# Optimization experiments

Measured on AMD Instinct MI355X. Metric: run time of the kernel, lower is better.

## Reference

```python
import jax, jax.numpy as jnp
import numpy as np

N_Q = 8
DIM = 128
CODEBOOK_SIZE = 1024


def setup_inputs() -> dict:
    key = jax.random.key(0)
    k1, k2 = jax.random.split(key)
    x = jax.random.normal(k1, (8, DIM, 4096), dtype=jnp.float32)
    codebooks = jax.random.normal(k2, (N_Q, CODEBOOK_SIZE, DIM), dtype=jnp.float32)
    return {"x": x, "codebooks": codebooks, "frame_rate": 75}


def _rvq(xt, codebooks):
    # xt: (B, T, D); codebooks: (n_q, K, D)
    def stage(carry, cb):
        residual, qout = carry
        # squared euclidean distance (B, T, K); argmin == Encodec's argmax of -dist
        d = (jnp.sum(residual * residual, axis=-1, keepdims=True)
             - 2.0 * jnp.einsum('btd,kd->btk', residual, cb)
             + jnp.sum(cb * cb, axis=-1))
        idx = jnp.argmin(d, axis=-1)                     # (B, T)
        q = cb[idx]                                       # gather: (B, T, D)
        # commit loss: mse(quantize.detach(), input)
        commit = jnp.mean((jax.lax.stop_gradient(q) - residual) ** 2)
        # straight-through estimator
        q_st = residual + jax.lax.stop_gradient(q - residual)
        return (residual - q_st, qout + q_st), (idx, commit)

    init = (xt, jnp.zeros_like(xt))
    (_, qout), (codes, commits) = jax.lax.scan(stage, init, codebooks)
    return qout, codes, commits


def reference(x, codebooks, frame_rate):
    # x: (B, D, T) -> (B, T, D)
    xt = jnp.swapaxes(x, 1, 2)
    qout, codes, commits = _rvq(xt, codebooks)
    quantized = jnp.swapaxes(qout, 1, 2)                 # (B, D, T)
    n_q, K, _ = codebooks.shape
    bw_per_q = np.log2(K) * frame_rate
    bw = jnp.asarray(n_q * bw_per_q, dtype=jnp.float32)
    penalty = jnp.mean(commits)
    return quantized, codes, bw, penalty
```

## Files before the change

kernel.cpp:

```cpp
#include <hip/hip_runtime.h>
#include <math.h>

#define Bsz 8
#define Dd  128
#define Tt  4096
#define Kk  1024
#define NQ  8
#define BT  (Bsz*Tt)
#define MT  128
#define NTHR 512
#define WV  8
#define DELTA 0.05f

typedef float f32x4 __attribute__((ext_vector_type(4)));
typedef short short8 __attribute__((ext_vector_type(8)));

__device__ __forceinline__ unsigned short f2bf(float x) {
    unsigned u = __float_as_uint(x);
    u += 0x7FFF + ((u >> 16) & 1);
    return (unsigned short)(u >> 16);
}
__device__ __forceinline__ float bf2f(unsigned short h) {
    return __uint_as_float(((unsigned)h) << 16);
}

__device__ __forceinline__ void gload_lds16(const void* g, void* l) {
    __builtin_amdgcn_global_load_lds(
        (const __attribute__((address_space(1))) unsigned int*)g,
        (__attribute__((address_space(3))) unsigned int*)l, 16, 0, 0);
}

__global__ void k_init(const float* __restrict__ x,
                       float* __restrict__ resid) {
    __shared__ float tile[32][33];
    int b  = blockIdx.z;
    int t0 = blockIdx.x * 32, d0 = blockIdx.y * 32;
    int tx = threadIdx.x, ty = threadIdx.y;
    #pragma unroll
    for (int k = 0; k < 4; k++) {
        int d = d0 + ty + k * 8;
        tile[ty + k * 8][tx] = x[((size_t)(b * Dd + d)) * Tt + t0 + tx];
    }
    __syncthreads();
    #pragma unroll
    for (int k = 0; k < 4; k++) {
        int t = t0 + ty + k * 8;
        resid[((size_t)(b * Tt + t)) * Dd + d0 + tx] = tile[tx][ty + k * 8];
    }
}

__global__ void k_prep(const float* __restrict__ cb, char* __restrict__ bswz) {
    int ln = threadIdx.x;
    int kc = blockIdx.x & 3;
    int t  = (blockIdx.x >> 2) & 63;
    int q  = blockIdx.x >> 8;
    int code = t * 16 + (ln & 15);
    int d0   = kc * 32 + (ln >> 4) * 8;
    const float* src = cb + ((size_t)(q * Kk + code)) * Dd + d0;
    float v[8];
    *(float4*)&v[0] = *(const float4*)src;
    *(float4*)&v[4] = *(const float4*)(src + 4);
    short8 h, l;
    #pragma unroll
    for (int j = 0; j < 8; j++) {
        unsigned short hu = f2bf(v[j]);
        h[j] = (short)hu;
        l[j] = (short)f2bf(v[j] - bf2f(hu));
    }
    char* base = bswz + ((size_t)(q * 64 + t)) * 8192;
    *(short8*)(base + kc * 1024 + ln * 16) = h;
    *(short8*)(base + 4096 + kc * 1024 + ln * 16) = l;
}

__global__ void k_c2(const float* __restrict__ cb,
                     float* __restrict__ c2,
                     double* __restrict__ commits) {
    int row  = blockIdx.x * 4 + (threadIdx.x >> 6);
    int lane = threadIdx.x & 63;
    const float* p = cb + (size_t)row * Dd;
    float a = p[lane], b = p[lane + 64];
    float s = a * a + b * b;
    #pragma unroll
    for (int off = 32; off; off >>= 1) s += __shfl_down(s, off);
    if (lane == 0) c2[row] = s;
    if (blockIdx.x == 0 && threadIdx.x < NQ) commits[threadIdx.x] = 0.0;
}

__device__ __forceinline__ float exact_score_sw(const float* __restrict__ rldsb,
                                                int p,
                                                const float* __restrict__ crow,
                                                float c2v) {
    const f32x4* r4 = (const f32x4*)rldsb;
    const f32x4* c4 = (const f32x4*)crow;
    int rb = p * 32, sw = p & 7;
    float a = 0.0f;
    #pragma unroll
    for (int d4 = 0; d4 < 32; d4++) {
        f32x4 r = r4[rb + (d4 ^ sw)];
        f32x4 c = c4[d4];
        a = fmaf(r[0], c[0], a); a = fmaf(r[1], c[1], a);
        a = fmaf(r[2], c[2], a); a = fmaf(r[3], c[3], a);
    }
    return fmaf(-2.0f, a, c2v);
}

__global__ __launch_bounds__(NTHR, 2) void k_rvq_fused(
        float* __restrict__ resid,
        const float* __restrict__ cb,
        const char*  __restrict__ bswz,
        const float* __restrict__ c2g,
        float* __restrict__ codes_f,
        double* __restrict__ commits) {
    __shared__ float rlds[MT * Dd];
    __shared__ float c2s[Kk];
    __shared__ f32x4 bbuf[2][2][512];
    __shared__ float fA1[MT], fA2[MT], fA3[MT];
    __shared__ float fB1[MT], fB2[MT], fB3[MT];
    __shared__ int   iA1[MT], iA2[MT], iB1[MT], iB2[MT];
    __shared__ int   sidxs[MT];
    __shared__ int   nfall, flist[MT];
    __shared__ float fwv[WV]; __shared__ int fwi[WV];
    __shared__ float csum[WV];

    const int tid  = threadIdx.x;
    const int w    = tid >> 6, ln = tid & 63;
    const int quad = ln >> 4,  m  = ln & 15;
    const int wg   = w & 3,    half = w >> 2;
    const int toff = half * 32;
    const int base = blockIdx.x * MT;
    const int prow0 = wg * 32 + m;
    const int prow1 = wg * 32 + 16 + m;

    f32x4* r4 = (f32x4*)rlds;

    {
        const f32x4* src = (const f32x4*)(resid + (size_t)base * Dd);
        #pragma unroll
        for (int i = 0; i < (MT * Dd / 4) / NTHR; i++) {
            int idx = tid + i * NTHR;
            int row = idx >> 5, c4 = idx & 31;
            r4[row * 32 + (c4 ^ (row & 7))] = src[idx];
        }
    }
    __syncthreads();

    #pragma unroll 1
    for (int q = 0; q < NQ; q++) {
        const float* cbq = cb + (size_t)q * Kk * Dd;
        const char*  bsq = bswz + (size_t)q * 64 * 8192;
        #pragma unroll
        for (int i = 0; i < Kk / NTHR; i++)
            c2s[tid + i * NTHR] = c2g[q * Kk + tid + i * NTHR];
        if (tid == 0) nfall = 0;

        short8 Ah0[4], Al0[4], Ah1[4], Al1[4];
        #pragma unroll
        for (int kc = 0; kc < 4; kc++) {
            int c4a = kc * 8 + quad * 2;
            float v[8];
            short8 h, l;
            *(f32x4*)&v[0] = r4[prow0 * 32 + (c4a ^ (prow0 & 7))];
            *(f32x4*)&v[4] = r4[prow0 * 32 + ((c4a + 1) ^ (prow0 & 7))];
            #pragma unroll
            for (int j = 0; j < 8; j++) {
                unsigned short hu = f2bf(v[j]);
                h[j] = (short)hu;
                l[j] = (short)f2bf(v[j] - bf2f(hu));
            }
            Ah0[kc] = h; Al0[kc] = l;
            *(f32x4*)&v[0] = r4[prow1 * 32 + (c4a ^ (prow1 & 7))];
            *(f32x4*)&v[4] = r4[prow1 * 32 + ((c4a + 1) ^ (prow1 & 7))];
            #pragma unroll
            for (int j = 0; j < 8; j++) {
                unsigned short hu = f2bf(v[j]);
                h[j] = (short)hu;
                l[j] = (short)f2bf(v[j] - bf2f(hu));
            }
            Ah1[kc] = h; Al1[kc] = l;
        }

        float b1a[4], b2a[4], b3a[4], b1b[4], b2b[4], b3b[4];
        int   i1a[4], i2a[4], i1b[4], i2b[4];
        #pragma unroll
        for (int j = 0; j < 4; j++) {
            b1a[j] = INFINITY; b2a[j] = INFINITY; b3a[j] = INFINITY;
            b1b[j] = INFINITY; b2b[j] = INFINITY; b3b[j] = INFINITY;
            i1a[j] = 0; i2a[j] = 0; i1b[j] = 0; i2b[j] = 0;
        }
        __syncthreads();

        gload_lds16(bsq + (size_t)toff * 0 + 0 * 8192 + w * 1024 + ln * 16,
                    (char*)&bbuf[0][0][0] + w * 1024);
        gload_lds16(bsq + (size_t)32 * 8192 + w * 1024 + ln * 16,
                    (char*)&bbuf[0][1][0] + w * 1024);
        int par = 0;

        #pragma unroll 1
        for (int s = 0; s < 32; s++) {
            asm volatile("s_waitcnt vmcnt(0)" ::: "memory");
            __builtin_amdgcn_s_barrier();
            __builtin_amdgcn_sched_barrier(0);
            if (s + 1 < 32) {
                gload_lds16(bsq + (size_t)(s + 1) * 8192 + w * 1024 + ln * 16,
                            (char*)&bbuf[par ^ 1][0][0] + w * 1024);
                gload_lds16(bsq + (size_t)(32 + s + 1) * 8192 + w * 1024 + ln * 16,
                            (char*)&bbuf[par ^ 1][1][0] + w * 1024);
            }
            const char* bb = (const char*)&bbuf[par][half][0];
            f32x4 a01a = {0.f,0.f,0.f,0.f}, a23a = {0.f,0.f,0.f,0.f};
            f32x4 a01b = {0.f,0.f,0.f,0.f}, a23b = {0.f,0.f,0.f,0.f};
            __builtin_amdgcn_s_setprio(1);
            #pragma unroll
            for (int kc = 0; kc < 4; kc++) {
                short8 ch = *(const short8*)(bb + kc * 1024 + ln * 16);
                short8 cl = *(const short8*)(bb + 4096 + kc * 1024 + ln * 16);
                if (kc < 2) {
                    a01a = __builtin_amdgcn_mfma_f32_16x16x32_bf16(Al0[kc], ch, a01a, 0, 0, 0);
                    a01a = __builtin_amdgcn_mfma_f32_16x16x32_bf16(Ah0[kc], cl, a01a, 0, 0, 0);
                    a01a = __builtin_amdgcn_mfma_f32_16x16x32_bf16(Ah0[kc], ch, a01a, 0, 0, 0);
                    a01b = __builtin_amdgcn_mfma_f32_16x16x32_bf16(Al1[kc], ch, a01b, 0, 0, 0);
                    a01b = __builtin_amdgcn_mfma_f32_16x16x32_bf16(Ah1[kc], cl, a01b, 0, 0, 0);
                    a01b = __builtin_amdgcn_mfma_f32_16x16x32_bf16(Ah1[kc], ch, a01b, 0, 0, 0);
                } else {
                    a23a = __builtin_amdgcn_mfma_f32_16x16x32_bf16(Al0[kc], ch, a23a, 0, 0, 0);
                    a23a = __builtin_amdgcn_mfma_f32_16x16x32_bf16(Ah0[kc], cl, a23a, 0, 0, 0);
                    a23a = __builtin_amdgcn_mfma_f32_16x16x32_bf16(Ah0[kc], ch, a23a, 0, 0, 0);
                    a23b = __builtin_amdgcn_mfma_f32_16x16x32_bf16(Al1[kc], ch, a23b, 0, 0, 0);
                    a23b = __builtin_amdgcn_mfma_f32_16x16x32_bf16(Ah1[kc], cl, a23b, 0, 0, 0);
                    a23b = __builtin_amdgcn_mfma_f32_16x16x32_bf16(Ah1[kc], ch, a23b, 0, 0, 0);
                }
            }
            __builtin_amdgcn_s_setprio(0);
            float c2v  = c2s[(toff + s) * 16 + m];
            int   code = (toff + s) * 16 + m;
            #pragma unroll
            for (int j = 0; j < 4; j++) {
                float sc = fmaf(-2.0f, a01a[j] + a23a[j], c2v);
                bool lt1 = sc < b1a[j];
                bool lt2 = sc < b2a[j];
                b3a[j] = __builtin_amdgcn_fmed3f(sc, b2a[j], b3a[j]);
                b2a[j] = __builtin_amdgcn_fmed3f(sc, b1a[j], b2a[j]);
                i2a[j] = lt1 ? i1a[j] : (lt2 ? code : i2a[j]);
                i1a[j] = lt1 ? code : i1a[j];
                b1a[j] = fminf(b1a[j], sc);
                float sd = fmaf(-2.0f, a01b[j] + a23b[j], c2v);
                bool mt1 = sd < b1b[j];
                bool mt2 = sd < b2b[j];
                b3b[j] = __builtin_amdgcn_fmed3f(sd, b2b[j], b3b[j]);
                b2b[j] = __builtin_amdgcn_fmed3f(sd, b1b[j], b2b[j]);
                i2b[j] = mt1 ? i1b[j] : (mt2 ? code : i2b[j]);
                i1b[j] = mt1 ? code : i1b[j];
                b1b[j] = fminf(b1b[j], sd);
            }
            asm volatile("s_waitcnt lgkmcnt(0)" ::: "memory");
            __builtin_amdgcn_sched_barrier(0);
            par ^= 1;
        }

        #pragma unroll
        for (int set = 0; set < 2; set++) {
            #pragma unroll
            for (int j = 0; j < 4; j++) {
                float v1 = set ? b1b[j] : b1a[j];
                float v2 = set ? b2b[j] : b2a[j];
                float v3 = set ? b3b[j] : b3a[j];
                int   a1 = set ? i1b[j] : i1a[j];
                int   a2 = set ? i2b[j] : i2a[j];
                #pragma unroll
                for (int off = 1; off < 16; off <<= 1) {
                    float w1 = __shfl_xor(v1, off); int j1 = __shfl_xor(a1, off);
                    float w2 = __shfl_xor(v2, off); int j2 = __shfl_xor(a2, off);
                    float w3 = __shfl_xor(v3, off);
                    bool aw = (v1 < w1) || (v1 == w1 && a1 < j1);
                    float x1 = aw ? v1 : w1, x2 = aw ? v2 : w2, x3 = aw ? v3 : w3;
                    int   y1 = aw ? a1 : j1, y2 = aw ? a2 : j2;
                    float z1 = aw ? w1 : v1, z2 = aw ? w2 : v2;
                    int   u1 = aw ? j1 : a1;
                    bool s2a = (x2 < z1) || (x2 == z1 && y2 < u1);
                    v1 = x1; a1 = y1;
                    v2 = s2a ? x2 : z1; a2 = s2a ? y2 : u1;
                    v3 = s2a ? fminf(x3, z1) : fminf(x2, z2);
                }
                if (m == 0) {
                    int p = wg * 32 + set * 16 + quad * 4 + j;
                    if (half == 0) {
                        fA1[p] = v1; fA2[p] = v2; fA3[p] = v3;
                        iA1[p] = a1; iA2[p] = a2;
                    } else {
                        fB1[p] = v1; fB2[p] = v2; fB3[p] = v3;
                        iB1[p] = a1; iB2[p] = a2;
                    }
                }
            }
        }
        __syncthreads();

        if (tid < MT) {
            int p = tid;
            float vA1 = fA1[p], vA2 = fA2[p], vA3 = fA3[p];
            int   aA1 = iA1[p], aA2 = iA2[p];
            float vB1 = fB1[p], vB2 = fB2[p], vB3 = fB3[p];
            int   aB1 = iB1[p], aB2 = iB2[p];
            bool aw = (vA1 < vB1) || (vA1 == vB1 && aA1 < aB1);
            float x1 = aw ? vA1 : vB1, x2 = aw ? vA2 : vB2, x3 = aw ? vA3 : vB3;
            int   y1 = aw ? aA1 : aB1, y2 = aw ? aA2 : aB2;
            float z1 = aw ? vB1 : vA1, z2 = aw ? vB2 : vA2;
            int   u1 = aw ? aB1 : aA1;
            bool s2a = (x2 < z1) || (x2 == z1 && y2 < u1);
            float v1 = x1;
            float v2 = s2a ? x2 : z1;
            float v3 = s2a ? fminf(x3, z1) : fminf(x2, z2);
            int   a1 = y1;
            int   a2 = s2a ? y2 : u1;
            if (v3 <= v1 + DELTA) {
                int sl = atomicAdd(&nfall, 1);
                flist[sl] = p;
            } else {
                int bk = a1;
                if (v2 <= v1 + DELTA) {
                    float s1 = exact_score_sw(rlds, p, cbq + (size_t)a1 * Dd, c2s[a1]);
                    float s2 = exact_score_sw(rlds, p, cbq + (size_t)a2 * Dd, c2s[a2]);
                    if (s2 < s1 || (s2 == s1 && a2 < a1)) bk = a2;
                }
                sidxs[p] = bk;
                codes_f[(size_t)q * BT + base + p] = (float)bk;
            }
        }
        __syncthreads();

        for (int fi = 0; fi < nfall; fi++) {
            int p = flist[fi];
            float bv = INFINITY; int bk = 0;
            #pragma unroll
            for (int c = 0; c < 2; c++) {
                int k = tid * 2 + c;
                float sc = exact_score_sw(rlds, p, cbq + (size_t)k * Dd, c2s[k]);
                if (sc < bv || (sc == bv && k < bk)) { bv = sc; bk = k; }
            }
            #pragma unroll
            for (int off = 32; off; off >>= 1) {
                float v2 = __shfl_xor(bv, off);
                int   k2 = __shfl_xor(bk, off);
                if (v2 < bv || (v2 == bv && k2 < bk)) { bv = v2; bk = k2; }
            }
            if (ln == 0) { fwv[w] = bv; fwi[w] = bk; }
            __syncthreads();
            if (tid == 0) {
                float v = fwv[0]; int k = fwi[0];
                #pragma unroll
                for (int w2 = 1; w2 < WV; w2++) {
                    if (fwv[w2] < v || (fwv[w2] == v && fwi[w2] < k)) {
                        v = fwv[w2]; k = fwi[w2];
                    }
                }
                sidxs[p] = k;
                codes_f[(size_t)q * BT + base + p] = (float)k;
            }
            __syncthreads();
        }
        __syncthreads();

        {
            int p = tid >> 2;
            int rb = p * 32, sw = p & 7, cb4 = (tid & 3) * 8;
            const float* qrow = cbq + ((size_t)sidxs[p]) * Dd + (tid & 3) * 32;
            float cacc = 0.0f;
            #pragma unroll
            for (int hh = 0; hh < 8; hh++) {
                f32x4 r  = r4[rb + ((cb4 + hh) ^ sw)];
                f32x4 qv = *(const f32x4*)(qrow + hh * 4);
                float t1x = qv[0] - r[0], t1y = qv[1] - r[1];
                float t1z = qv[2] - r[2], t1w = qv[3] - r[3];
                float qsx = r[0] + t1x, qsy = r[1] + t1y;
                float qsz = r[2] + t1z, qsw = r[3] + t1w;
                f32x4 nr = { r[0] - qsx, r[1] - qsy, r[2] - qsz, r[3] - qsw };
                r4[rb + ((cb4 + hh) ^ sw)] = nr;
                cacc = fmaf(t1x, t1x, cacc); cacc = fmaf(t1y, t1y, cacc);
                cacc = fmaf(t1z, t1z, cacc); cacc = fmaf(t1w, t1w, cacc);
            }
            #pragma unroll
            for (int off = 32; off; off >>= 1) cacc += __shfl_down(cacc, off);
            if (ln == 0) csum[w] = cacc;
        }
        __syncthreads();
        if (tid == 0) {
            double sd = 0.0;
            #pragma unroll
            for (int w2 = 0; w2 < WV; w2++) sd += (double)csum[w2];
            atomicAdd(commits + q, sd);
        }
        __syncthreads();
    }

    {
        f32x4* dst = (f32x4*)(resid + (size_t)base * Dd);
        #pragma unroll
        for (int i = 0; i < (MT * Dd / 4) / NTHR; i++) {
            int idx = tid + i * NTHR;
            int row = idx >> 5, c4 = idx & 31;
            dst[idx] = r4[row * 32 + (c4 ^ (row & 7))];
        }
    }
}

__global__ void k_final(const float* __restrict__ x,
                        const float* __restrict__ resid,
                        float* __restrict__ outq) {
    __shared__ float tile[32][33];
    int b  = blockIdx.z;
    int t0 = blockIdx.x * 32, d0 = blockIdx.y * 32;
    int tx = threadIdx.x, ty = threadIdx.y;
    #pragma unroll
    for (int k = 0; k < 4; k++) {
        int t = t0 + ty + k * 8;
        tile[ty + k * 8][tx] = resid[((size_t)(b * Tt + t)) * Dd + d0 + tx];
    }
    __syncthreads();
    #pragma unroll
    for (int k = 0; k < 4; k++) {
        int d = d0 + ty + k * 8;
        size_t o = ((size_t)(b * Dd + d)) * Tt + t0 + tx;
        outq[o] = x[o] - tile[tx][ty + k * 8];
    }
}

__global__ void k_scalars(const double* __restrict__ commits,
                          const int* __restrict__ frame_rate,
                          float* __restrict__ outs) {
    if (threadIdx.x == 0 && blockIdx.x == 0) {
        double s = 0.0;
        #pragma unroll
        for (int q = 0; q < NQ; q++) s += commits[q];
        double per_elem = s / ((double)NQ * (double)BT * (double)Dd);
        outs[0] = (float)(NQ * 10.0 * (double)frame_rate[0]);
        outs[1] = (float)per_elem;
    }
}

extern "C" void kernel_launch(void* const* d_in, const int* in_sizes, int n_in,
                              void* d_out, int out_size, void* d_ws, size_t ws_size,
                              hipStream_t stream) {
    const float* x  = (const float*)d_in[0];
    const float* cb = (const float*)d_in[1];
    const int*   fr = (const int*)d_in[2];

    float* outq    = (float*)d_out;
    float* codes_f = outq + (size_t)Bsz * Dd * Tt;
    float* scal    = codes_f + (size_t)NQ * BT;

    char* ws = (char*)d_ws;
    float*  resid   = (float*)ws;
    float*  c2      = resid + (size_t)BT * Dd;
    double* commits = (double*)(c2 + (size_t)NQ * Kk);
    char*   bswz    = (char*)(commits + NQ);

    dim3 tb(32, 8, 1);
    k_init<<<dim3(Tt / 32, Dd / 32, Bsz), tb, 0, stream>>>(x, resid);
    k_prep<<<NQ * 256, 64, 0, stream>>>(cb, bswz);
    k_c2<<<NQ * Kk / 4, 256, 0, stream>>>(cb, c2, commits);

    k_rvq_fused<<<BT / MT, NTHR, 0, stream>>>(resid, cb, bswz, c2,
                                              codes_f, commits);

    k_final<<<dim3(Tt / 32, Dd / 32, Bsz), tb, 0, stream>>>(x, resid, outq);
    k_scalars<<<1, 64, 0, stream>>>(commits, fr, scal);
}
```

Baseline: 560.7 us.

## Drop bf16 residual low part, pack code indices into scores, adaptive rescore window

```diff
diff --git a/kernel.cpp b/kernel.cpp
--- a/kernel.cpp
+++ b/kernel.cpp
@@ -10,7 +10,6 @@
 #define MT  128
 #define NTHR 512
 #define WV  8
-#define DELTA 0.05f
 
 typedef float f32x4 __attribute__((ext_vector_type(4)));
 typedef short short8 __attribute__((ext_vector_type(8)));
@@ -22,12 +21,6 @@
 }
 __device__ __forceinline__ float bf2f(unsigned short h) {
     return __uint_as_float(((unsigned)h) << 16);
-}
-
-__device__ __forceinline__ void gload_lds16(const void* g, void* l) {
-    __builtin_amdgcn_global_load_lds(
-        (const __attribute__((address_space(1))) unsigned int*)g,
-        (__attribute__((address_space(3))) unsigned int*)l, 16, 0, 0);
 }
 
 __global__ void k_init(const float* __restrict__ x,
@@ -74,6 +67,7 @@
 
 __global__ void k_c2(const float* __restrict__ cb,
                      float* __restrict__ c2,
+                     unsigned* __restrict__ cmax2u,
                      double* __restrict__ commits) {
     int row  = blockIdx.x * 4 + (threadIdx.x >> 6);
     int lane = threadIdx.x & 63;
@@ -82,7 +76,10 @@
     float s = a * a + b * b;
     #pragma unroll
     for (int off = 32; off; off >>= 1) s += __shfl_down(s, off);
-    if (lane == 0) c2[row] = s;
+    if (lane == 0) {
+        c2[row] = s;
+        atomicMax(&cmax2u[row >> 10], __float_as_uint(s));
+    }
     if (blockIdx.x == 0 && threadIdx.x < NQ) commits[threadIdx.x] = 0.0;
 }
 
@@ -104,19 +101,20 @@
     return fmaf(-2.0f, a, c2v);
 }
 
-__global__ __launch_bounds__(NTHR, 2) void k_rvq_fused(
+__global__ __launch_bounds__(NTHR, 1) void k_rvq_fused(
         float* __restrict__ resid,
         const float* __restrict__ cb,
         const char*  __restrict__ bswz,
         const float* __restrict__ c2g,
+        const unsigned* __restrict__ cmax2u,
         float* __restrict__ codes_f,
         double* __restrict__ commits) {
     __shared__ float rlds[MT * Dd];
     __shared__ float c2s[Kk];
     __shared__ f32x4 bbuf[2][2][512];
+    __shared__ float winp[MT];
     __shared__ float fA1[MT], fA2[MT], fA3[MT];
     __shared__ float fB1[MT], fB2[MT], fB3[MT];
-    __shared__ int   iA1[MT], iA2[MT], iB1[MT], iB2[MT];
     __shared__ int   sidxs[MT];
     __shared__ int   nfall, flist[MT];
     __shared__ float fwv[WV]; __shared__ int fwi[WV];
@@ -126,7 +124,6 @@
     const int w    = tid >> 6, ln = tid & 63;
     const int quad = ln >> 4,  m  = ln & 15;
     const int wg   = w & 3,    half = w >> 2;
-    const int toff = half * 32;
     const int base = blockIdx.x * MT;
     const int prow0 = wg * 32 + m;
     const int prow1 = wg * 32 + 16 + m;
@@ -142,118 +139,124 @@
             r4[row * 32 + (c4 ^ (row & 7))] = src[idx];
         }
     }
+    {
+        const f32x4* B0 = (const f32x4*)bswz;
+        bbuf[0][0][tid] = B0[tid];
+        bbuf[0][1][tid] = B0[tid + 32 * 512];
+    }
+    int par = 0;
     __syncthreads();
 
     #pragma unroll 1
     for (int q = 0; q < NQ; q++) {
         const float* cbq = cb + (size_t)q * Kk * Dd;
-        const char*  bsq = bswz + (size_t)q * 64 * 8192;
         #pragma unroll
         for (int i = 0; i < Kk / NTHR; i++)
             c2s[tid + i * NTHR] = c2g[q * Kk + tid + i * NTHR];
         if (tid == 0) nfall = 0;
-
-        short8 Ah0[4], Al0[4], Ah1[4], Al1[4];
+        float cmaxq = sqrtf(__uint_as_float(cmax2u[q]));
+
+        short8 Ah0[4], Ah1[4];
+        float r2p0 = 0.0f, r2p1 = 0.0f;
         #pragma unroll
         for (int kc = 0; kc < 4; kc++) {
             int c4a = kc * 8 + quad * 2;
             float v[8];
-            short8 h, l;
+            short8 h;
             *(f32x4*)&v[0] = r4[prow0 * 32 + (c4a ^ (prow0 & 7))];
             *(f32x4*)&v[4] = r4[prow0 * 32 + ((c4a + 1) ^ (prow0 & 7))];
             #pragma unroll
             for (int j = 0; j < 8; j++) {
-                unsigned short hu = f2bf(v[j]);
-                h[j] = (short)hu;
-                l[j] = (short)f2bf(v[j] - bf2f(hu));
-            }
-            Ah0[kc] = h; Al0[kc] = l;
+                h[j] = (short)f2bf(v[j]);
+                r2p0 = fmaf(v[j], v[j], r2p0);
+            }
+            Ah0[kc] = h;
             *(f32x4*)&v[0] = r4[prow1 * 32 + (c4a ^ (prow1 & 7))];
             *(f32x4*)&v[4] = r4[prow1 * 32 + ((c4a + 1) ^ (prow1 & 7))];
             #pragma unroll
             for (int j = 0; j < 8; j++) {
-                unsigned short hu = f2bf(v[j]);
-                h[j] = (short)hu;
-                l[j] = (short)f2bf(v[j] - bf2f(hu));
-            }
-            Ah1[kc] = h; Al1[kc] = l;
+                h[j] = (short)f2bf(v[j]);
+                r2p1 = fmaf(v[j], v[j], r2p1);
+            }
+            Ah1[kc] = h;
+        }
+        r2p0 += __shfl_xor(r2p0, 16); r2p0 += __shfl_xor(r2p0, 32);
+        r2p1 += __shfl_xor(r2p1, 16); r2p1 += __shfl_xor(r2p1, 32);
+        {
+            float R0 = sqrtf(r2p0), R1 = sqrtf(r2p1);
+            float sb0 = fmaf(2.0f * R0, cmaxq, cmaxq * cmaxq);
+            float sb1 = fmaf(2.0f * R1, cmaxq, cmaxq * cmaxq);
+            float p20 = exp2f(ceilf(log2f(fmaxf(sb0, 2.0f))));
+            float p21 = exp2f(ceilf(log2f(fmaxf(sb1, 2.0f))));
+            float w0 = fmaf(0.016f * R0, cmaxq, 0.06f) + p20 * (1.0f/4096.0f);
+            float w1 = fmaf(0.016f * R1, cmaxq, 0.06f) + p21 * (1.0f/4096.0f);
+            if (quad == 0) { winp[prow0] = w0; winp[prow1] = w1; }
         }
 
         float b1a[4], b2a[4], b3a[4], b1b[4], b2b[4], b3b[4];
-        int   i1a[4], i2a[4], i1b[4], i2b[4];
         #pragma unroll
         for (int j = 0; j < 4; j++) {
             b1a[j] = INFINITY; b2a[j] = INFINITY; b3a[j] = INFINITY;
             b1b[j] = INFINITY; b2b[j] = INFINITY; b3b[j] = INFINITY;
-            i1a[j] = 0; i2a[j] = 0; i1b[j] = 0; i2b[j] = 0;
-        }
-        __syncthreads();
-
-        gload_lds16(bsq + (size_t)toff * 0 + 0 * 8192 + w * 1024 + ln * 16,
-                    (char*)&bbuf[0][0][0] + w * 1024);
-        gload_lds16(bsq + (size_t)32 * 8192 + w * 1024 + ln * 16,
-                    (char*)&bbuf[0][1][0] + w * 1024);
-        int par = 0;
+        }
+        __syncthreads();
 
         #pragma unroll 1
         for (int s = 0; s < 32; s++) {
-            asm volatile("s_waitcnt vmcnt(0)" ::: "memory");
-            __builtin_amdgcn_s_barrier();
-            __builtin_amdgcn_sched_barrier(0);
-            if (s + 1 < 32) {
-                gload_lds16(bsq + (size_t)(s + 1) * 8192 + w * 1024 + ln * 16,
-                            (char*)&bbuf[par ^ 1][0][0] + w * 1024);
-                gload_lds16(bsq + (size_t)(32 + s + 1) * 8192 + w * 1024 + ln * 16,
-                            (char*)&bbuf[par ^ 1][1][0] + w * 1024);
+            const int pidx = q * 32 + s + 1;
+            const bool hs = (pidx < NQ * 32);
+            f32x4 stg0, stg1;
+            if (hs) {
+                int nq = pidx >> 5, ns = pidx & 31;
+                const f32x4* Bn =
+                    (const f32x4*)(bswz + ((size_t)(nq * 64 + ns)) * 8192);
+                stg0 = Bn[tid];
+                stg1 = Bn[tid + 32 * 512];
             }
             const char* bb = (const char*)&bbuf[par][half][0];
-            f32x4 a01a = {0.f,0.f,0.f,0.f}, a23a = {0.f,0.f,0.f,0.f};
-            f32x4 a01b = {0.f,0.f,0.f,0.f}, a23b = {0.f,0.f,0.f,0.f};
+            f32x4 a01A = {0.f,0.f,0.f,0.f}, a23A = {0.f,0.f,0.f,0.f};
+            f32x4 a01B = {0.f,0.f,0.f,0.f}, a23B = {0.f,0.f,0.f,0.f};
             __builtin_amdgcn_s_setprio(1);
             #pragma unroll
             for (int kc = 0; kc < 4; kc++) {
                 short8 ch = *(const short8*)(bb + kc * 1024 + ln * 16);
                 short8 cl = *(const short8*)(bb + 4096 + kc * 1024 + ln * 16);
                 if (kc < 2) {
-                    a01a = __builtin_amdgcn_mfma_f32_16x16x32_bf16(Al0[kc], ch, a01a, 0, 0, 0);
-                    a01a = __builtin_amdgcn_mfma_f32_16x16x32_bf16(Ah0[kc], cl, a01a, 0, 0, 0);
-                    a01a = __builtin_amdgcn_mfma_f32_16x16x32_bf16(Ah0[kc], ch, a01a, 0, 0, 0);
-                    a01b = __builtin_amdgcn_mfma_f32_16x16x32_bf16(Al1[kc], ch, a01b, 0, 0, 0);
-                    a01b = __builtin_amdgcn_mfma_f32_16x16x32_bf16(Ah1[kc], cl, a01b, 0, 0, 0);
-                    a01b = __builtin_amdgcn_mfma_f32_16x16x32_bf16(Ah1[kc], ch, a01b, 0, 0, 0);
+                    a01A = __builtin_amdgcn_mfma_f32_16x16x32_bf16(Ah0[kc], ch, a01A, 0, 0, 0);
+                    a01A = __builtin_amdgcn_mfma_f32_16x16x32_bf16(Ah0[kc], cl, a01A, 0, 0, 0);
+                    a01B = __builtin_amdgcn_mfma_f32_16x16x32_bf16(Ah1[kc], ch, a01B, 0, 0, 0);
+                    a01B = __builtin_amdgcn_mfma_f32_16x16x32_bf16(Ah1[kc], cl, a01B, 0, 0, 0);
                 } else {
-                    a23a = __builtin_amdgcn_mfma_f32_16x16x32_bf16(Al0[kc], ch, a23a, 0, 0, 0);
-                    a23a = __builtin_amdgcn_mfma_f32_16x16x32_bf16(Ah0[kc], cl, a23a, 0, 0, 0);
-                    a23a = __builtin_amdgcn_mfma_f32_16x16x32_bf16(Ah0[kc], ch, a23a, 0, 0, 0);
-                    a23b = __builtin_amdgcn_mfma_f32_16x16x32_bf16(Al1[kc], ch, a23b, 0, 0, 0);
-                    a23b = __builtin_amdgcn_mfma_f32_16x16x32_bf16(Ah1[kc], cl, a23b, 0, 0, 0);
-                    a23b = __builtin_amdgcn_mfma_f32_16x16x32_bf16(Ah1[kc], ch, a23b, 0, 0, 0);
+                    a23A = __builtin_amdgcn_mfma_f32_16x16x32_bf16(Ah0[kc], ch, a23A, 0, 0, 0);
+                    a23A = __builtin_amdgcn_mfma_f32_16x16x32_bf16(Ah0[kc], cl, a23A, 0, 0, 0);
+                    a23B = __builtin_amdgcn_mfma_f32_16x16x32_bf16(Ah1[kc], ch, a23B, 0, 0, 0);
+                    a23B = __builtin_amdgcn_mfma_f32_16x16x32_bf16(Ah1[kc], cl, a23B, 0, 0, 0);
                 }
             }
             __builtin_amdgcn_s_setprio(0);
-            float c2v  = c2s[(toff + s) * 16 + m];
-            int   code = (toff + s) * 16 + m;
+            const int codei = half * 512 + s * 16 + m;
+            float c2v = c2s[codei];
+            const unsigned codeu = (unsigned)codei;
             #pragma unroll
             for (int j = 0; j < 4; j++) {
-                float sc = fmaf(-2.0f, a01a[j] + a23a[j], c2v);
-                bool lt1 = sc < b1a[j];
-                bool lt2 = sc < b2a[j];
-                b3a[j] = __builtin_amdgcn_fmed3f(sc, b2a[j], b3a[j]);
-                b2a[j] = __builtin_amdgcn_fmed3f(sc, b1a[j], b2a[j]);
-                i2a[j] = lt1 ? i1a[j] : (lt2 ? code : i2a[j]);
-                i1a[j] = lt1 ? code : i1a[j];
-                b1a[j] = fminf(b1a[j], sc);
-                float sd = fmaf(-2.0f, a01b[j] + a23b[j], c2v);
-                bool mt1 = sd < b1b[j];
-                bool mt2 = sd < b2b[j];
-                b3b[j] = __builtin_amdgcn_fmed3f(sd, b2b[j], b3b[j]);
-                b2b[j] = __builtin_amdgcn_fmed3f(sd, b1b[j], b2b[j]);
-                i2b[j] = mt1 ? i1b[j] : (mt2 ? code : i2b[j]);
-                i1b[j] = mt1 ? code : i1b[j];
-                b1b[j] = fminf(b1b[j], sd);
-            }
-            asm volatile("s_waitcnt lgkmcnt(0)" ::: "memory");
-            __builtin_amdgcn_sched_barrier(0);
+                float sA = fmaf(-2.0f, a01A[j] + a23A[j], c2v);
+                float pA = __uint_as_float(
+                    (__float_as_uint(sA) & 0xFFFFFC00u) | codeu);
+                b3a[j] = __builtin_amdgcn_fmed3f(pA, b2a[j], b3a[j]);
+                b2a[j] = __builtin_amdgcn_fmed3f(pA, b1a[j], b2a[j]);
+                b1a[j] = fminf(b1a[j], pA);
+                float sB = fmaf(-2.0f, a01B[j] + a23B[j], c2v);
+                float pB = __uint_as_float(
+                    (__float_as_uint(sB) & 0xFFFFFC00u) | codeu);
+                b3b[j] = __builtin_amdgcn_fmed3f(pB, b2b[j], b3b[j]);
+                b2b[j] = __builtin_amdgcn_fmed3f(pB, b1b[j], b2b[j]);
+                b1b[j] = fminf(b1b[j], pB);
+            }
+            if (hs) {
+                bbuf[par ^ 1][0][tid] = stg0;
+                bbuf[par ^ 1][1][tid] = stg1;
+            }
+            __syncthreads();
             par ^= 1;
         }
 
@@ -264,32 +267,23 @@
                 float v1 = set ? b1b[j] : b1a[j];
                 float v2 = set ? b2b[j] : b2a[j];
                 float v3 = set ? b3b[j] : b3a[j];
-                int   a1 = set ? i1b[j] : i1a[j];
-                int   a2 = set ? i2b[j] : i2a[j];
                 #pragma unroll
                 for (int off = 1; off < 16; off <<= 1) {
-                    float w1 = __shfl_xor(v1, off); int j1 = __shfl_xor(a1, off);
-                    float w2 = __shfl_xor(v2, off); int j2 = __shfl_xor(a2, off);
+                    float w1 = __shfl_xor(v1, off);
+                    float w2 = __shfl_xor(v2, off);
                     float w3 = __shfl_xor(v3, off);
-                    bool aw = (v1 < w1) || (v1 == w1 && a1 < j1);
-                    float x1 = aw ? v1 : w1, x2 = aw ? v2 : w2, x3 = aw ? v3 : w3;
-                    int   y1 = aw ? a1 : j1, y2 = aw ? a2 : j2;
+                    bool aw = v1 < w1;
+                    float x2 = aw ? v2 : w2, x3 = aw ? v3 : w3;
                     float z1 = aw ? w1 : v1, z2 = aw ? w2 : v2;
-                    int   u1 = aw ? j1 : a1;
-                    bool s2a = (x2 < z1) || (x2 == z1 && y2 < u1);
-                    v1 = x1; a1 = y1;
-                    v2 = s2a ? x2 : z1; a2 = s2a ? y2 : u1;
-                    v3 = s2a ? fminf(x3, z1) : fminf(x2, z2);
+                    v1 = fminf(v1, w1);
+                    bool s2 = x2 < z1;
+                    v2 = fminf(x2, z1);
+                    v3 = s2 ? fminf(x3, z1) : fminf(x2, z2);
                 }
                 if (m == 0) {
                     int p = wg * 32 + set * 16 + quad * 4 + j;
-                    if (half == 0) {
-                        fA1[p] = v1; fA2[p] = v2; fA3[p] = v3;
-                        iA1[p] = a1; iA2[p] = a2;
-                    } else {
-                        fB1[p] = v1; fB2[p] = v2; fB3[p] = v3;
-                        iB1[p] = a1; iB2[p] = a2;
-                    }
+                    if (half == 0) { fA1[p] = v1; fA2[p] = v2; fA3[p] = v3; }
+                    else           { fB1[p] = v1; fB2[p] = v2; fB3[p] = v3; }
                 }
             }
         }
@@ -298,29 +292,26 @@
         if (tid < MT) {
             int p = tid;
             float vA1 = fA1[p], vA2 = fA2[p], vA3 = fA3[p];
-            int   aA1 = iA1[p], aA2 = iA2[p];
             float vB1 = fB1[p], vB2 = fB2[p], vB3 = fB3[p];
-            int   aB1 = iB1[p], aB2 = iB2[p];
-            bool aw = (vA1 < vB1) || (vA1 == vB1 && aA1 < aB1);
-            float x1 = aw ? vA1 : vB1, x2 = aw ? vA2 : vB2, x3 = aw ? vA3 : vB3;
-            int   y1 = aw ? aA1 : aB1, y2 = aw ? aA2 : aB2;
+            bool aw = vA1 < vB1;
+            float x2 = aw ? vA2 : vB2, x3 = aw ? vA3 : vB3;
             float z1 = aw ? vB1 : vA1, z2 = aw ? vB2 : vA2;
-            int   u1 = aw ? aB1 : aA1;
-            bool s2a = (x2 < z1) || (x2 == z1 && y2 < u1);
-            float v1 = x1;
-            float v2 = s2a ? x2 : z1;
-            float v3 = s2a ? fminf(x3, z1) : fminf(x2, z2);
-            int   a1 = y1;
-            int   a2 = s2a ? y2 : u1;
-            if (v3 <= v1 + DELTA) {
+            float v1 = fminf(vA1, vB1);
+            bool s2 = x2 < z1;
+            float v2 = fminf(x2, z1);
+            float v3 = s2 ? fminf(x3, z1) : fminf(x2, z2);
+            int a1 = (int)(__float_as_uint(v1) & 1023u);
+            int a2 = (int)(__float_as_uint(v2) & 1023u);
+            float win = winp[p];
+            if (v3 <= v1 + win) {
                 int sl = atomicAdd(&nfall, 1);
                 flist[sl] = p;
             } else {
                 int bk = a1;
-                if (v2 <= v1 + DELTA) {
+                if (v2 <= v1 + win) {
                     float s1 = exact_score_sw(rlds, p, cbq + (size_t)a1 * Dd, c2s[a1]);
-                    float s2 = exact_score_sw(rlds, p, cbq + (size_t)a2 * Dd, c2s[a2]);
-                    if (s2 < s1 || (s2 == s1 && a2 < a1)) bk = a2;
+                    float s2e = exact_score_sw(rlds, p, cbq + (size_t)a2 * Dd, c2s[a2]);
+                    if (s2e < s1 || (s2e == s1 && a2 < a1)) bk = a2;
                 }
                 sidxs[p] = bk;
                 codes_f[(size_t)q * BT + base + p] = (float)bk;
@@ -449,17 +440,20 @@
     float* scal    = codes_f + (size_t)NQ * BT;
 
     char* ws = (char*)d_ws;
-    float*  resid   = (float*)ws;
-    float*  c2      = resid + (size_t)BT * Dd;
-    double* commits = (double*)(c2 + (size_t)NQ * Kk);
-    char*   bswz    = (char*)(commits + NQ);
+    float*    resid   = (float*)ws;
+    float*    c2      = resid + (size_t)BT * Dd;
+    double*   commits = (double*)(c2 + (size_t)NQ * Kk);
+    unsigned* cmax2u  = (unsigned*)(commits + NQ);
+    char*     bswz    = (char*)(cmax2u + NQ + 2);
+
+    hipMemsetAsync(cmax2u, 0, NQ * sizeof(unsigned), stream);
 
     dim3 tb(32, 8, 1);
     k_init<<<dim3(Tt / 32, Dd / 32, Bsz), tb, 0, stream>>>(x, resid);
     k_prep<<<NQ * 256, 64, 0, stream>>>(cb, bswz);
-    k_c2<<<NQ * Kk / 4, 256, 0, stream>>>(cb, c2, commits);
-
-    k_rvq_fused<<<BT / MT, NTHR, 0, stream>>>(resid, cb, bswz, c2,
+    k_c2<<<NQ * Kk / 4, 256, 0, stream>>>(cb, c2, cmax2u, commits);
+
+    k_rvq_fused<<<BT / MT, NTHR, 0, stream>>>(resid, cb, bswz, c2, cmax2u,
                                               codes_f, commits);
 
     k_final<<<dim3(Tt / 32, Dd / 32, Bsz), tb, 0, stream>>>(x, resid, outq);
```

Measured after the change: 1.261 ms. +124.8%, slower.
